# Kernel tuning notes

Measured on AMD Instinct MI355X. Metric: run time of the kernel, lower is better.

Reference implementation:

```python
import jax, jax.numpy as jnp
import numpy as np

EMBED_DIM = 1024
NUM_HEADS = 4
HEAD_DIM = EMBED_DIM // NUM_HEADS  # 256
QKV_DIM = 64                        # NUM_HEADS * QKV_DIM == HEAD_DIM (required by the residual add)
B, S = 16, 4096


def setup_inputs() -> dict:
    key = jax.random.key(0)
    kx, kq, kk, kv = jax.random.split(key, 4)
    x = jax.random.normal(kx, (B, S, EMBED_DIM), dtype=jnp.float32)
    # torch nn.Linear weights have shape [out_features, in_features]; y = x @ W.T
    scale = 1.0 / np.sqrt(HEAD_DIM)
    W_q = jax.random.normal(kq, (QKV_DIM, HEAD_DIM), dtype=jnp.float32) * scale
    W_k = jax.random.normal(kk, (QKV_DIM, HEAD_DIM), dtype=jnp.float32) * scale
    W_v = jax.random.normal(kv, (QKV_DIM, HEAD_DIM), dtype=jnp.float32) * scale
    return {"x": x, "W_q": W_q, "W_k": W_k, "W_v": W_v}


def reference(x, W_q, W_k, W_v):
    b = x.shape[0]
    # [B, S, H, Dh] -> [B, H, S, Dh]
    xh = x.reshape(b, -1, NUM_HEADS, HEAD_DIM).transpose(0, 2, 1, 3)
    # Shared projections applied per head (vectorized over the head axis)
    Q = jnp.einsum('bhsd,qd->bhsq', xh, W_q)  # [B,H,S,Qk]
    K = jnp.einsum('bhsd,qd->bhsq', xh, W_k)
    V = jnp.einsum('bhsd,qd->bhsq', xh, W_v)
    # Nonstandard ordering from the original: scores = Q^T K over the sequence axis
    attn_scores = jnp.einsum('bhsq,bhsk->bhqk', Q, K) / np.sqrt(HEAD_DIM)  # [B,H,Qk,Qk]
    attn_weights = jax.nn.softmax(attn_scores, axis=-1)
    # attn_output is computed in the original but NOT used in the returned value
    attn_output = jnp.einsum('bhsq,bhqk->bhsk', V, attn_weights)  # dead code, DCE'd under jit
    del attn_output
    # cat(V per head, dim=-1) -> [B, S, H*Qk];  x_head is the LAST head's slice [B, S, Dh]
    V_cat = V.transpose(0, 2, 1, 3).reshape(b, -1, NUM_HEADS * QKV_DIM)
    x_last_head = xh[:, NUM_HEADS - 1]  # [B, S, Dh]
    return x_last_head + V_cat
```

## Files before the change

### kernel.cpp

```cpp
#include <hip/hip_runtime.h>
#include <hip/hip_bf16.h>


#define NTOK (16 * 4096)

typedef short bf16x8 __attribute__((ext_vector_type(8)));
typedef float f32x4 __attribute__((ext_vector_type(4)));

__device__ __forceinline__ short f2bf(float f) {
    __hip_bfloat16 h = __float2bfloat16(f);
    return __builtin_bit_cast(short, h);
}

__device__ __forceinline__ int wofs(int q, int d) {
    return (((q << 9) | (d << 1)) ^ ((q & 7) << 4));
}

__global__ __launch_bounds__(256, 4) void mha_vcat_kernel(
    const float* __restrict__ x, const float* __restrict__ Wv,
    float* __restrict__ out)
{
    __shared__ char Wlds[64 * 256 * 2];

    const int tid = threadIdx.x;

    #pragma unroll
    for (int i = 0; i < 8; ++i) {
        const int flat = i * 2048 + tid * 8;
        const f32x4 lo = *reinterpret_cast<const f32x4*>(Wv + flat);
        const f32x4 hi = *reinterpret_cast<const f32x4*>(Wv + flat + 4);
        bf16x8 wb;
        wb[0] = f2bf(lo[0]); wb[1] = f2bf(lo[1]); wb[2] = f2bf(lo[2]); wb[3] = f2bf(lo[3]);
        wb[4] = f2bf(hi[0]); wb[5] = f2bf(hi[1]); wb[6] = f2bf(hi[2]); wb[7] = f2bf(hi[3]);
        *reinterpret_cast<bf16x8*>(Wlds + wofs(flat >> 8, flat & 255)) = wb;
    }
    __syncthreads();

    const int wid  = tid >> 6;
    const int lane = tid & 63;
    const int cl   = lane & 15;
    const int g    = lane >> 4;

    const long tokBase = (long)blockIdx.x * 64 + wid * 16;
    const float* rowp = x + (tokBase + cl) * 1024;

    bf16x8 diag0, diag1;
    #pragma unroll
    for (int j = 0; j < 8; ++j) {
        diag0[j] = (g * 8 + j == cl)      ? f2bf(1.0f) : (short)0;
        diag1[j] = (g * 8 + j == cl + 16) ? f2bf(1.0f) : (short)0;
    }

    f32x4 acc[4][4];
    #pragma unroll
    for (int h = 0; h < 4; ++h)
        #pragma unroll
        for (int n = 0; n < 4; ++n)
            acc[h][n] = (f32x4){0.f, 0.f, 0.f, 0.f};

    #pragma unroll
    for (int kk = 0; kk < 8; ++kk) {
        bf16x8 xfr[4];
        #pragma unroll
        for (int h = 0; h < 4; ++h) {
            const float* p = rowp + h * 256 + kk * 32 + g * 8;
            const f32x4 lo = *reinterpret_cast<const f32x4*>(p);
            const f32x4 hi = *reinterpret_cast<const f32x4*>(p + 4);
            xfr[h][0] = f2bf(lo[0]); xfr[h][1] = f2bf(lo[1]);
            xfr[h][2] = f2bf(lo[2]); xfr[h][3] = f2bf(lo[3]);
            xfr[h][4] = f2bf(hi[0]); xfr[h][5] = f2bf(hi[1]);
            xfr[h][6] = f2bf(hi[2]); xfr[h][7] = f2bf(hi[3]);
        }
        bf16x8 wfr[4];
        #pragma unroll
        for (int n = 0; n < 4; ++n)
            wfr[n] = *reinterpret_cast<const bf16x8*>(
                Wlds + wofs(n * 16 + cl, kk * 32 + g * 8));

        #pragma unroll
        for (int h = 0; h < 4; ++h)
            #pragma unroll
            for (int n = 0; n < 4; ++n)
                acc[h][n] = __builtin_amdgcn_mfma_f32_16x16x32_bf16(
                    wfr[n], xfr[h], acc[h][n], 0, 0, 0);

        const int n0 = 2 * kk, n1 = 2 * kk + 1;
        acc[n0 >> 2][n0 & 3] = __builtin_amdgcn_mfma_f32_16x16x32_bf16(
            diag0, xfr[3], acc[n0 >> 2][n0 & 3], 0, 0, 0);
        acc[n1 >> 2][n1 & 3] = __builtin_amdgcn_mfma_f32_16x16x32_bf16(
            diag1, xfr[3], acc[n1 >> 2][n1 & 3], 0, 0, 0);
    }

    float* trow = out + (tokBase + cl) * 256;
    #pragma unroll
    for (int h = 0; h < 4; ++h)
        #pragma unroll
        for (int n = 0; n < 4; ++n)
            *reinterpret_cast<f32x4*>(trow + h * 64 + n * 16 + g * 4) = acc[h][n];
}

extern "C" void kernel_launch(void* const* d_in, const int* in_sizes, int n_in,
                              void* d_out, int out_size, void* d_ws, size_t ws_size,
                              hipStream_t stream) {
    const float* x  = (const float*)d_in[0];
    const float* Wv = (const float*)d_in[3];
    float* out = (float*)d_out;
    mha_vcat_kernel<<<dim3(NTOK / 64), dim3(256), 0, stream>>>(x, Wv, out);
}
```

Before: 76.72 us.

## Stage x through double-buffered LDS with register-resident weights and per-wave head split

Each block now handles 128 tokens in 8 chunks of 16. Every chunk is loaded with coalesced full-row global reads, converted to bf16 and staged into a swizzled, double-buffered LDS tile, with the next chunk's loads issued before the current chunk's MFMAs. The weight fragments are held in registers for the whole block instead of being reread from LDS, and each wave computes one head's output. This targets strided, uncoalesced per-lane x loads and poor load/compute overlap, at the cost of high register pressure (launch bounds drop to 1 block per SM), fewer blocks, and two barriers per chunk.

```diff
diff --git a/kernel.cpp b/kernel.cpp
--- a/kernel.cpp
+++ b/kernel.cpp
@@ -2,47 +2,67 @@
 #include <hip/hip_bf16.h>
 
 
-#define NTOK (16 * 4096)
+#define TOKENS_PER_BLOCK 128
+#define NCHUNK 8
+#define NBLOCKS (16 * 4096 / TOKENS_PER_BLOCK)
 
+typedef short bf16x4 __attribute__((ext_vector_type(4)));
 typedef short bf16x8 __attribute__((ext_vector_type(8)));
-typedef float f32x4 __attribute__((ext_vector_type(4)));
+typedef float f32x4  __attribute__((ext_vector_type(4)));
 
 __device__ __forceinline__ short f2bf(float f) {
     __hip_bfloat16 h = __float2bfloat16(f);
     return __builtin_bit_cast(short, h);
 }
-
-__device__ __forceinline__ int wofs(int q, int d) {
-    return (((q << 9) | (d << 1)) ^ ((q & 7) << 4));
+__device__ __forceinline__ bf16x4 cvt4(f32x4 a) {
+    bf16x4 r;
+    r[0] = f2bf(a[0]); r[1] = f2bf(a[1]); r[2] = f2bf(a[2]); r[3] = f2bf(a[3]);
+    return r;
+}
+__device__ __forceinline__ bf16x8 cvt8(f32x4 a, f32x4 b) {
+    bf16x8 r;
+    r[0] = f2bf(a[0]); r[1] = f2bf(a[1]); r[2] = f2bf(a[2]); r[3] = f2bf(a[3]);
+    r[4] = f2bf(b[0]); r[5] = f2bf(b[1]); r[6] = f2bf(b[2]); r[7] = f2bf(b[3]);
+    return r;
 }
 
-__global__ __launch_bounds__(256, 4) void mha_vcat_kernel(
+__device__ __forceinline__ int xofs(int tok, int colbyte) {
+    return tok * 2048 + (colbyte ^ ((tok & 7) << 4));
+}
+
+__global__ __launch_bounds__(256, 1) void mha_vcat_kernel(
     const float* __restrict__ x, const float* __restrict__ Wv,
     float* __restrict__ out)
 {
-    __shared__ char Wlds[64 * 256 * 2];
+    __shared__ char X[2][16 * 2048];
 
-    const int tid = threadIdx.x;
-
-    #pragma unroll
-    for (int i = 0; i < 8; ++i) {
-        const int flat = i * 2048 + tid * 8;
-        const f32x4 lo = *reinterpret_cast<const f32x4*>(Wv + flat);
-        const f32x4 hi = *reinterpret_cast<const f32x4*>(Wv + flat + 4);
-        bf16x8 wb;
-        wb[0] = f2bf(lo[0]); wb[1] = f2bf(lo[1]); wb[2] = f2bf(lo[2]); wb[3] = f2bf(lo[3]);
-        wb[4] = f2bf(hi[0]); wb[5] = f2bf(hi[1]); wb[6] = f2bf(hi[2]); wb[7] = f2bf(hi[3]);
-        *reinterpret_cast<bf16x8*>(Wlds + wofs(flat >> 8, flat & 255)) = wb;
-    }
-    __syncthreads();
-
+    const int tid  = threadIdx.x;
     const int wid  = tid >> 6;
     const int lane = tid & 63;
     const int cl   = lane & 15;
     const int g    = lane >> 4;
 
-    const long tokBase = (long)blockIdx.x * 64 + wid * 16;
-    const float* rowp = x + (tokBase + cl) * 1024;
+    const long blockTok = (long)blockIdx.x * TOKENS_PER_BLOCK;
+
+    const int srow  = tid >> 7;
+    const int scolA = (tid & 127) * 4;
+
+    f32x4 sA[8], sB[8];
+    #pragma unroll
+    for (int p = 0; p < 8; ++p) {
+        const float* q = x + (blockTok + p * 2 + srow) * 1024;
+        sA[p] = *(const f32x4*)(q + scolA);
+        sB[p] = *(const f32x4*)(q + 512 + scolA);
+    }
+
+    bf16x8 wfr[8][4];
+    #pragma unroll
+    for (int kk = 0; kk < 8; ++kk)
+        #pragma unroll
+        for (int n = 0; n < 4; ++n) {
+            const float* q = Wv + (n * 16 + cl) * 256 + kk * 32 + g * 8;
+            wfr[kk][n] = cvt8(*(const f32x4*)q, *(const f32x4*)(q + 4));
+        }
 
     bf16x8 diag0, diag1;
     #pragma unroll
@@ -51,52 +71,66 @@
         diag1[j] = (g * 8 + j == cl + 16) ? f2bf(1.0f) : (short)0;
     }
 
-    f32x4 acc[4][4];
     #pragma unroll
-    for (int h = 0; h < 4; ++h)
+    for (int p = 0; p < 8; ++p) {
+        const int lt = p * 2 + srow;
+        *(bf16x4*)(&X[0][xofs(lt, scolA * 2)])        = cvt4(sA[p]);
+        *(bf16x4*)(&X[0][xofs(lt, 1024 + scolA * 2)]) = cvt4(sB[p]);
+    }
+    __syncthreads();
+
+    #pragma unroll
+    for (int c = 0; c < NCHUNK; ++c) {
+        if (c < NCHUNK - 1) {
+            #pragma unroll
+            for (int p = 0; p < 8; ++p) {
+                const float* q = x + (blockTok + (c + 1) * 16 + p * 2 + srow) * 1024;
+                sA[p] = *(const f32x4*)(q + scolA);
+                sB[p] = *(const f32x4*)(q + 512 + scolA);
+            }
+        }
+
+        const char* Xb = X[c & 1];
+        f32x4 acc[4];
+        #pragma unroll
+        for (int n = 0; n < 4; ++n) acc[n] = (f32x4){0.f, 0.f, 0.f, 0.f};
+
+        #pragma unroll
+        for (int kk = 0; kk < 8; ++kk) {
+            const bf16x8 xf = *(const bf16x8*)(
+                Xb + xofs(cl, wid * 512 + kk * 64 + g * 16));
+            #pragma unroll
+            for (int n = 0; n < 4; ++n)
+                acc[n] = __builtin_amdgcn_mfma_f32_16x16x32_bf16(
+                    wfr[kk][n], xf, acc[n], 0, 0, 0);
+        }
+        #pragma unroll
+        for (int s = 0; s < 2; ++s) {
+            const bf16x8 x3 = *(const bf16x8*)(
+                Xb + xofs(cl, 1536 + wid * 128 + s * 64 + g * 16));
+            acc[2 * s]     = __builtin_amdgcn_mfma_f32_16x16x32_bf16(
+                diag0, x3, acc[2 * s], 0, 0, 0);
+            acc[2 * s + 1] = __builtin_amdgcn_mfma_f32_16x16x32_bf16(
+                diag1, x3, acc[2 * s + 1], 0, 0, 0);
+        }
+
+        float* trow = out + (blockTok + c * 16 + cl) * 256 + wid * 64;
         #pragma unroll
         for (int n = 0; n < 4; ++n)
-            acc[h][n] = (f32x4){0.f, 0.f, 0.f, 0.f};
+            *(f32x4*)(trow + n * 16 + g * 4) = acc[n];
 
-    #pragma unroll
-    for (int kk = 0; kk < 8; ++kk) {
-        bf16x8 xfr[4];
-        #pragma unroll
-        for (int h = 0; h < 4; ++h) {
-            const float* p = rowp + h * 256 + kk * 32 + g * 8;
-            const f32x4 lo = *reinterpret_cast<const f32x4*>(p);
-            const f32x4 hi = *reinterpret_cast<const f32x4*>(p + 4);
-            xfr[h][0] = f2bf(lo[0]); xfr[h][1] = f2bf(lo[1]);
-            xfr[h][2] = f2bf(lo[2]); xfr[h][3] = f2bf(lo[3]);
-            xfr[h][4] = f2bf(hi[0]); xfr[h][5] = f2bf(hi[1]);
-            xfr[h][6] = f2bf(hi[2]); xfr[h][7] = f2bf(hi[3]);
+        if (c < NCHUNK - 1) {
+            __syncthreads();
+            char* Xn = X[(c + 1) & 1];
+            #pragma unroll
+            for (int p = 0; p < 8; ++p) {
+                const int lt = p * 2 + srow;
+                *(bf16x4*)(&Xn[xofs(lt, scolA * 2)])        = cvt4(sA[p]);
+                *(bf16x4*)(&Xn[xofs(lt, 1024 + scolA * 2)]) = cvt4(sB[p]);
+            }
+            __syncthreads();
         }
-        bf16x8 wfr[4];
-        #pragma unroll
-        for (int n = 0; n < 4; ++n)
-            wfr[n] = *reinterpret_cast<const bf16x8*>(
-                Wlds + wofs(n * 16 + cl, kk * 32 + g * 8));
-
-        #pragma unroll
-        for (int h = 0; h < 4; ++h)
-            #pragma unroll
-            for (int n = 0; n < 4; ++n)
-                acc[h][n] = __builtin_amdgcn_mfma_f32_16x16x32_bf16(
-                    wfr[n], xfr[h], acc[h][n], 0, 0, 0);
-
-        const int n0 = 2 * kk, n1 = 2 * kk + 1;
-        acc[n0 >> 2][n0 & 3] = __builtin_amdgcn_mfma_f32_16x16x32_bf16(
-            diag0, xfr[3], acc[n0 >> 2][n0 & 3], 0, 0, 0);
-        acc[n1 >> 2][n1 & 3] = __builtin_amdgcn_mfma_f32_16x16x32_bf16(
-            diag1, xfr[3], acc[n1 >> 2][n1 & 3], 0, 0, 0);
     }
-
-    float* trow = out + (tokBase + cl) * 256;
-    #pragma unroll
-    for (int h = 0; h < 4; ++h)
-        #pragma unroll
-        for (int n = 0; n < 4; ++n)
-            *reinterpret_cast<f32x4*>(trow + h * 64 + n * 16 + g * 4) = acc[h][n];
 }
 
 extern "C" void kernel_launch(void* const* d_in, const int* in_sizes, int n_in,
@@ -105,5 +139,5 @@
     const float* x  = (const float*)d_in[0];
     const float* Wv = (const float*)d_in[3];
     float* out = (float*)d_out;
-    mha_vcat_kernel<<<dim3(NTOK / 64), dim3(256), 0, stream>>>(x, Wv, out);
+    mha_vcat_kernel<<<dim3(NBLOCKS), dim3(256), 0, stream>>>(x, Wv, out);
 }
```

Result: slower. 82.32 us (+7.3%).
